# Kernel optimization log

Hardware: AMD Instinct MI355X
Metric: run time of the kernel (lower is better)

The kernel has to match this reference:

```python
import jax, jax.numpy as jnp
import numpy as np

D_MODEL = 2048
NUM_HEADS = 16
HEAD_DIM = D_MODEL // NUM_HEADS


def setup_inputs() -> dict:
    key = jax.random.key(0)
    ks = jax.random.split(key, 11)
    B, S = 2, 2048
    scale = 1.0 / np.sqrt(D_MODEL)
    inp = {
        "q": jax.random.normal(ks[0], (B, S, D_MODEL), jnp.float32),
        "k": jax.random.normal(ks[1], (B, S, D_MODEL), jnp.float32),
        "v": jax.random.normal(ks[2], (B, S, D_MODEL), jnp.float32),
        "Wq": jax.random.normal(ks[3], (D_MODEL, D_MODEL), jnp.float32) * scale,
        "bq": jnp.zeros((D_MODEL,), jnp.float32),
        "Wk": jax.random.normal(ks[4], (D_MODEL, D_MODEL), jnp.float32) * scale,
        "bk": jnp.zeros((D_MODEL,), jnp.float32),
        "Wv": jax.random.normal(ks[5], (D_MODEL, D_MODEL), jnp.float32) * scale,
        "bv": jnp.zeros((D_MODEL,), jnp.float32),
        "Wo": jax.random.normal(ks[6], (D_MODEL, D_MODEL), jnp.float32) * scale,
        "bo": jnp.zeros((D_MODEL,), jnp.float32),
    }
    return inp


def reference(q, k, v, Wq, bq, Wk, bk, Wv, bv, Wo, bo):
    B, S, _ = q.shape
    # projections (torch Linear: x @ W.T + b)
    qh = (q @ Wq.T + bq).reshape(B, S, NUM_HEADS, HEAD_DIM).transpose(0, 2, 1, 3)
    kh = (k @ Wk.T + bk).reshape(B, S, NUM_HEADS, HEAD_DIM).transpose(0, 2, 1, 3)
    vh = (v @ Wv.T + bv).reshape(B, S, NUM_HEADS, HEAD_DIM).transpose(0, 2, 1, 3)
    # scaled dot-product attention, full O(S^2) scores as in original
    scores = jnp.einsum("bhqd,bhkd->bhqk", qh, kh) / jnp.sqrt(
        jnp.asarray(HEAD_DIM, jnp.float32)
    )
    attn = jax.nn.softmax(scores, axis=-1)
    out = jnp.einsum("bhqk,bhkd->bhqd", attn, vh)
    out = out.transpose(0, 2, 1, 3).reshape(B, S, D_MODEL)
    return out @ Wo.T + bo
```

## Files before the change

### kernel.cpp

```cpp
#include <hip/hip_runtime.h>


typedef __attribute__((ext_vector_type(8))) short bf16x8;
typedef __attribute__((ext_vector_type(4))) float f32x4;
typedef __attribute__((ext_vector_type(8))) unsigned short u16x8;

__device__ __forceinline__ unsigned short f2bf(float f) {
  unsigned int u = __float_as_uint(f);
  u += 0x7fffu + ((u >> 16) & 1u);
  return (unsigned short)(u >> 16);
}

#if __has_builtin(__builtin_amdgcn_cvt_pk_bf16_f32)
__device__ __forceinline__ unsigned int pack2bf(float x, float y) {
  auto r = __builtin_amdgcn_cvt_pk_bf16_f32(x, y);
  return __builtin_bit_cast(unsigned int, r);
}
#else
__device__ __forceinline__ unsigned int pack2bf(float x, float y) {
  return (unsigned int)f2bf(x) | ((unsigned int)f2bf(y) << 16);
}
#endif

__device__ __forceinline__ float fast_exp2(float x) {
#if __has_builtin(__builtin_amdgcn_exp2f)
  return __builtin_amdgcn_exp2f(x);
#else
  return exp2f(x);
#endif
}

__device__ __forceinline__ void async16(const void* g, void* l) {
  __builtin_amdgcn_global_load_lds(
      (const __attribute__((address_space(1))) unsigned int*)g,
      (__attribute__((address_space(3))) unsigned int*)l, 16, 0, 0);
}

__device__ __forceinline__ f32x4 mfma_bf16(bf16x8 a, bf16x8 b, f32x4 c) {
  return __builtin_amdgcn_mfma_f32_16x16x32_bf16(a, b, c, 0, 0, 0);
}

__global__ __launch_bounds__(256) void cvt_kernel(
    const float* __restrict__ q, const float* __restrict__ k,
    const float* __restrict__ v, const float* __restrict__ Wq,
    const float* __restrict__ Wk, const float* __restrict__ Wv,
    const float* __restrict__ Wo, unsigned short* __restrict__ Xq,
    unsigned short* __restrict__ Xk, unsigned short* __restrict__ Xv,
    unsigned short* __restrict__ WqB, unsigned short* __restrict__ WkB,
    unsigned short* __restrict__ WvB, unsigned short* __restrict__ WoB) {
  size_t i = ((size_t)blockIdx.x * 256 + threadIdx.x) * 8;
  const float* src;
  unsigned short* dst;
  size_t off;
  if (i < 8388608ull) { src = q; dst = Xq; off = i; }
  else if (i < 16777216ull) { src = k; dst = Xk; off = i - 8388608ull; }
  else if (i < 25165824ull) { src = v; dst = Xv; off = i - 16777216ull; }
  else if (i < 29360128ull) { src = Wq; dst = WqB; off = i - 25165824ull; }
  else if (i < 33554432ull) { src = Wk; dst = WkB; off = i - 29360128ull; }
  else if (i < 37748736ull) { src = Wv; dst = WvB; off = i - 33554432ull; }
  else { src = Wo; dst = WoB; off = i - 37748736ull; }
  f32x4 a = *(const f32x4*)(src + off);
  f32x4 b = *(const f32x4*)(src + off + 4);
  u16x8 r;
  r[0] = f2bf(a[0]); r[1] = f2bf(a[1]); r[2] = f2bf(a[2]); r[3] = f2bf(a[3]);
  r[4] = f2bf(b[0]); r[5] = f2bf(b[1]); r[6] = f2bf(b[2]); r[7] = f2bf(b[3]);
  *(u16x8*)(dst + off) = r;
}

__device__ __forceinline__ void gemm_core_k2048(
    const unsigned short* __restrict__ A, const unsigned short* __restrict__ Bm,
    int m0, int n0, unsigned short* As, unsigned short* Bs,
    f32x4 (&acc)[4][4]) {
  const int tid = threadIdx.x;
  const int lane = tid & 63;
  const int wave = tid >> 6;
  const int quad = lane >> 4;
  const int l15 = lane & 15;
  const int wmt = (wave >> 1) * 4;
  const int wnt = (wave & 1) * 4;
  const int K = 2048;

  auto stage = [&](int kt, int buf) {
    unsigned short* SA = As + buf * (128 * 64);
    unsigned short* SB = Bs + buf * (128 * 64);
#pragma unroll
    for (int p = 0; p < 4; ++p) {
      int x = p * 256 + tid;
      int row = ((x >> 7) << 4) + ((x >> 3) & 15);
      int gk = kt + (((x & 7) ^ ((x >> 3) & 7)) << 3);
      async16(A + (size_t)(m0 + row) * K + gk,
              (char*)SA + (size_t)(p * 256 + wave * 64) * 16);
      async16(Bm + (size_t)(n0 + row) * K + gk,
              (char*)SB + (size_t)(p * 256 + wave * 64) * 16);
    }
  };
  stage(0, 0);
#pragma unroll 1
  for (int it = 0; it < 32; ++it) {
    __syncthreads();
    if (it + 1 < 32) stage((it + 1) * 64, (it + 1) & 1);
    const unsigned short* SA = As + (it & 1) * (128 * 64);
    const unsigned short* SB = Bs + (it & 1) * (128 * 64);
#pragma unroll
    for (int s = 0; s < 2; ++s) {
      const int cs = (s * 4 + quad) ^ (l15 & 7);
      bf16x8 af[4], bfr[4];
#pragma unroll
      for (int t = 0; t < 4; ++t) {
        af[t] = *(const bf16x8*)(SA + ((wmt + t) * 128 + l15 * 8 + cs) * 8);
        bfr[t] = *(const bf16x8*)(SB + ((wnt + t) * 128 + l15 * 8 + cs) * 8);
      }
#pragma unroll
      for (int mt = 0; mt < 4; ++mt)
#pragma unroll
        for (int nt = 0; nt < 4; ++nt)
          acc[mt][nt] = mfma_bf16(af[mt], bfr[nt], acc[mt][nt]);
    }
  }
}

__global__ __launch_bounds__(256, 2) void qkv_gemm(
    const unsigned short* __restrict__ Xq, const unsigned short* __restrict__ Xk,
    const unsigned short* __restrict__ Xv, const unsigned short* __restrict__ Wq,
    const unsigned short* __restrict__ Wk, const unsigned short* __restrict__ Wv,
    const float* __restrict__ bq, const float* __restrict__ bk,
    const float* __restrict__ bv, unsigned short* __restrict__ Qb,
    unsigned short* __restrict__ Kb, unsigned short* __restrict__ Vt) {
  __shared__ unsigned short As[2][128 * 64];
  __shared__ unsigned short Bs[2][128 * 64];
  const int z = blockIdx.z;
  const unsigned short* A = z == 0 ? Xq : z == 1 ? Xk : Xv;
  const unsigned short* Bm = z == 0 ? Wq : z == 1 ? Wk : Wv;
  const float* bias = z == 0 ? bq : z == 1 ? bk : bv;
  const int m0 = blockIdx.y * 128;
  const int n0 = blockIdx.x * 128;

  f32x4 acc[4][4];
#pragma unroll
  for (int i = 0; i < 4; ++i)
#pragma unroll
    for (int j = 0; j < 4; ++j) acc[i][j] = f32x4{0.f, 0.f, 0.f, 0.f};
  gemm_core_k2048(A, Bm, m0, n0, As[0], Bs[0], acc);

  const int lane = threadIdx.x & 63;
  const int wave = threadIdx.x >> 6;
  const int quad = lane >> 4;
  const int l15 = lane & 15;
  const int wmt = (wave >> 1) * 4;
  const int wnt = (wave & 1) * 4;
  const float SK = z == 0 ? 0.12753102331285527f : 1.0f;
  const int N = 2048;

#pragma unroll
  for (int nt = 0; nt < 4; ++nt) {
    int col = n0 + (wnt + nt) * 16 + l15;
    float bv_ = bias[col];
    if (z == 2) {
      int h = col >> 7, d = col & 127;
#pragma unroll
      for (int mt = 0; mt < 4; ++mt) {
        int row0 = m0 + (wmt + mt) * 16 + quad * 4;
        int bb = row0 >> 11, s = row0 & 2047;
        uint2 pk;
        pk.x = pack2bf(acc[mt][nt][0] + bv_, acc[mt][nt][1] + bv_);
        pk.y = pack2bf(acc[mt][nt][2] + bv_, acc[mt][nt][3] + bv_);
        *(uint2*)(Vt + ((size_t)((bb * 16 + h) * 128 + d)) * 2048 + s) = pk;
      }
    } else {
      unsigned short* C = z == 0 ? Qb : Kb;
#pragma unroll
      for (int mt = 0; mt < 4; ++mt) {
        int row0 = m0 + (wmt + mt) * 16 + quad * 4;
#pragma unroll
        for (int r = 0; r < 4; ++r)
          C[(size_t)(row0 + r) * N + col] = f2bf((acc[mt][nt][r] + bv_) * SK);
      }
    }
  }
}

__global__ __launch_bounds__(256, 2) void o_gemm(
    const unsigned short* __restrict__ A, const unsigned short* __restrict__ Bm,
    const float* __restrict__ bias, float* __restrict__ Cf) {
  __shared__ unsigned short As[2][128 * 64];
  __shared__ unsigned short Bs[2][128 * 64];
  const int m0 = blockIdx.y * 128;
  const int n0 = blockIdx.x * 128;

  f32x4 acc[4][4];
#pragma unroll
  for (int i = 0; i < 4; ++i)
#pragma unroll
    for (int j = 0; j < 4; ++j) acc[i][j] = f32x4{0.f, 0.f, 0.f, 0.f};
  gemm_core_k2048(A, Bm, m0, n0, As[0], Bs[0], acc);

  const int lane = threadIdx.x & 63;
  const int wave = threadIdx.x >> 6;
  const int quad = lane >> 4;
  const int l15 = lane & 15;
  const int wmt = (wave >> 1) * 4;
  const int wnt = (wave & 1) * 4;
  const int N = 2048;
#pragma unroll
  for (int nt = 0; nt < 4; ++nt) {
    int col = n0 + (wnt + nt) * 16 + l15;
    float bv_ = bias[col];
#pragma unroll
    for (int mt = 0; mt < 4; ++mt) {
      int row0 = m0 + (wmt + mt) * 16 + quad * 4;
#pragma unroll
      for (int r = 0; r < 4; ++r)
        Cf[(size_t)(row0 + r) * N + col] = acc[mt][nt][r] + bv_;
    }
  }
}

__global__ __launch_bounds__(256, 2) void attn_kernel(
    const unsigned short* __restrict__ Qg, const unsigned short* __restrict__ Kg,
    const unsigned short* __restrict__ Vt, unsigned short* __restrict__ ctx) {
  __shared__ unsigned short Ks[2][64 * 128];
  __shared__ unsigned short Vs[2][128 * 64];
  __shared__ unsigned short Ps[128 * 64];
  const int tid = threadIdx.x;
  const int lane = tid & 63;
  const int wave = tid >> 6;
  const int quad = lane >> 4;
  const int l15 = lane & 15;
  const int qt = blockIdx.x, h = blockIdx.y, b = blockIdx.z;
  const int q0 = qt * 128;
  const int swz = (l15 & 7) * 8;

  bf16x8 aq[2][4];
#pragma unroll
  for (int mt = 0; mt < 2; ++mt) {
    const unsigned short* qrow =
        Qg + (size_t)(b * 2048 + q0 + wave * 32 + mt * 16 + l15) * 2048 + h * 128;
#pragma unroll
    for (int ks = 0; ks < 4; ++ks)
      aq[mt][ks] = *(const bf16x8*)(qrow + ks * 32 + quad * 8);
  }

  f32x4 o[2][8];
#pragma unroll
  for (int mt = 0; mt < 2; ++mt)
#pragma unroll
    for (int dt = 0; dt < 8; ++dt) o[mt][dt] = f32x4{0.f, 0.f, 0.f, 0.f};
  f32x4 lacc[2] = {f32x4{0.f, 0.f, 0.f, 0.f}, f32x4{0.f, 0.f, 0.f, 0.f}};

  auto stage = [&](int t, int buf) {
#pragma unroll
    for (int p = 0; p < 4; ++p) {
      int slot = p * 256 + tid;
      {
        int nt = slot >> 8, c = (slot >> 4) & 15, r15 = slot & 15;
        const unsigned short* g =
            Kg + (size_t)(b * 2048 + t * 64 + nt * 16 + r15) * 2048 + h * 128 + c * 8;
        async16(g, (char*)Ks[buf] + (size_t)(p * 256 + wave * 64) * 16);
      }
      {
        int dt = slot >> 7, c = (slot >> 4) & 7, n15 = slot & 15;
        const unsigned short* g =
            Vt + ((size_t)(b * 16 + h) * 128 + dt * 16 + n15) * 2048 + t * 64 + c * 8;
        async16(g, (char*)Vs[buf] + (size_t)(p * 256 + wave * 64) * 16);
      }
    }
  };
  stage(0, 0);

  for (int t = 0; t < 32; ++t) {
    __syncthreads();
    if (t + 1 < 32) stage(t + 1, (t + 1) & 1);
    const unsigned short* Kb = Ks[t & 1];
    const unsigned short* Vb = Vs[t & 1];

    f32x4 sc[2][4];
#pragma unroll
    for (int nt = 0; nt < 4; ++nt) {
      sc[0][nt] = f32x4{0.f, 0.f, 0.f, 0.f};
      sc[1][nt] = f32x4{0.f, 0.f, 0.f, 0.f};
#pragma unroll
      for (int ks = 0; ks < 4; ++ks) {
        bf16x8 bk = *(const bf16x8*)(Kb + (nt * 256 + (ks * 4 + quad) * 16 + l15) * 8);
        sc[0][nt] = mfma_bf16(bk, aq[0][ks], sc[0][nt]);
        sc[1][nt] = mfma_bf16(bk, aq[1][ks], sc[1][nt]);
      }
    }

#pragma unroll
    for (int mt = 0; mt < 2; ++mt) {
      int prow = (wave * 32 + mt * 16 + l15) * 64;
#pragma unroll
      for (int nt = 0; nt < 4; ++nt) {
        f32x4 p;
#pragma unroll
        for (int r = 0; r < 4; ++r) p[r] = fast_exp2(sc[mt][nt][r]);
        lacc[mt] += p;
        uint2 pk;
        pk.x = pack2bf(p[0], p[1]);
        pk.y = pack2bf(p[2], p[3]);
        *(uint2*)(Ps + prow + ((nt * 16 + quad * 4) ^ swz)) = pk;
      }
    }

    bf16x8 ap[2][2];
#pragma unroll
    for (int mt = 0; mt < 2; ++mt) {
      int prow = (wave * 32 + mt * 16 + l15) * 64;
#pragma unroll
      for (int ks = 0; ks < 2; ++ks)
        ap[mt][ks] = *(const bf16x8*)(Ps + prow + ((ks * 32 + quad * 8) ^ swz));
    }
#pragma unroll
    for (int dt = 0; dt < 8; ++dt) {
#pragma unroll
      for (int ks = 0; ks < 2; ++ks) {
        bf16x8 bv = *(const bf16x8*)(Vb + (dt * 128 + (ks * 4 + quad) * 16 + l15) * 8);
        o[0][dt] = mfma_bf16(ap[0][ks], bv, o[0][dt]);
        o[1][dt] = mfma_bf16(ap[1][ks], bv, o[1][dt]);
      }
    }
  }

  float lq[2];
#pragma unroll
  for (int mt = 0; mt < 2; ++mt) {
    float s = lacc[mt][0] + lacc[mt][1] + lacc[mt][2] + lacc[mt][3];
    s += __shfl_xor(s, 16, 64);
    s += __shfl_xor(s, 32, 64);
    lq[mt] = s;
  }

#pragma unroll
  for (int mt = 0; mt < 2; ++mt) {
#pragma unroll
    for (int r = 0; r < 4; ++r) {
      float lr = __shfl(lq[mt], quad * 4 + r, 64);
      float inv = 1.0f / lr;
      unsigned short* crow =
          ctx + (size_t)(b * 2048 + q0 + wave * 32 + mt * 16 + quad * 4 + r) * 2048 +
          h * 128;
#pragma unroll
      for (int dt = 0; dt < 8; ++dt)
        crow[dt * 16 + l15] = f2bf(o[mt][dt][r] * inv);
    }
  }
}

extern "C" void kernel_launch(void* const* d_in, const int* in_sizes, int n_in,
                              void* d_out, int out_size, void* d_ws,
                              size_t ws_size, hipStream_t stream) {
  const float* q = (const float*)d_in[0];
  const float* k = (const float*)d_in[1];
  const float* v = (const float*)d_in[2];
  const float* Wq = (const float*)d_in[3];
  const float* bq = (const float*)d_in[4];
  const float* Wk = (const float*)d_in[5];
  const float* bk = (const float*)d_in[6];
  const float* Wv = (const float*)d_in[7];
  const float* bv = (const float*)d_in[8];
  const float* Wo = (const float*)d_in[9];
  const float* bo = (const float*)d_in[10];
  float* out = (float*)d_out;

  char* ws = (char*)d_ws;
  const size_t MB = 1024 * 1024;
  unsigned short* Xq  = (unsigned short*)(ws + 0 * MB);
  unsigned short* Xk  = (unsigned short*)(ws + 16 * MB);
  unsigned short* Xv  = (unsigned short*)(ws + 32 * MB);
  unsigned short* WqB = (unsigned short*)(ws + 48 * MB);
  unsigned short* WkB = (unsigned short*)(ws + 56 * MB);
  unsigned short* WvB = (unsigned short*)(ws + 64 * MB);
  unsigned short* WoB = (unsigned short*)(ws + 72 * MB);
  unsigned short* Qb  = (unsigned short*)(ws + 80 * MB);
  unsigned short* Kb  = (unsigned short*)(ws + 96 * MB);
  unsigned short* Vt  = (unsigned short*)(ws + 112 * MB);
  unsigned short* ctx = Xq;

  cvt_kernel<<<20480, 256, 0, stream>>>(q, k, v, Wq, Wk, Wv, Wo, Xq, Xk, Xv,
                                        WqB, WkB, WvB, WoB);
  qkv_gemm<<<dim3(16, 32, 3), 256, 0, stream>>>(Xq, Xk, Xv, WqB, WkB, WvB, bq,
                                                bk, bv, Qb, Kb, Vt);
  attn_kernel<<<dim3(16, 16, 2), 256, 0, stream>>>(Qb, Kb, Vt, ctx);
  o_gemm<<<dim3(16, 32), 256, 0, stream>>>(ctx, WoB, bo, out);
}
```

Measured before the change: 452.9 us.

## Replace QKV projection GEMM with 256x256-tile, 8-wave pipelined kernel

The QKV projection kernel now uses 256x256 output tiles with 512 threads, in place of 128x128 tiles with 256 threads. The K-loop is software-pipelined: global loads for four 128-row sub-tiles are staggered across phases, LDS fragment reads are double-buffered in registers, and MFMA phases are raised in priority with setprio. The aim is more data reuse per LDS byte, less global traffic, and memory latency hidden behind MFMA work. In exchange, the grid shrinks to 384 blocks, register pressure from 128 accumulators is high, and the per-phase barriers add synchronization overhead.

```diff
diff --git a/kernel.cpp b/kernel.cpp
--- a/kernel.cpp
+++ b/kernel.cpp
@@ -67,6 +67,184 @@
   *(u16x8*)(dst + off) = r;
 }
 
+#define MFMA_PHASE(AF, MB)                                                    \
+  do {                                                                        \
+    __builtin_amdgcn_s_setprio(1);                                            \
+    _Pragma("unroll") for (int ks = 0; ks < 2; ++ks) {                        \
+      _Pragma("unroll") for (int m2 = 0; m2 < 2; ++m2) {                      \
+        _Pragma("unroll") for (int nt = 0; nt < 4; ++nt) {                    \
+          acc[(MB) + m2][nt] =                                                \
+              mfma_bf16(AF[m2][ks], Bf[nt][ks], acc[(MB) + m2][nt]);          \
+        }                                                                     \
+      }                                                                       \
+    }                                                                         \
+    __builtin_amdgcn_s_setprio(0);                                            \
+  } while (0)
+
+__global__ __launch_bounds__(512, 2) void qkv_gemm256(
+    const unsigned short* __restrict__ Xq, const unsigned short* __restrict__ Xk,
+    const unsigned short* __restrict__ Xv, const unsigned short* __restrict__ Wq,
+    const unsigned short* __restrict__ Wk, const unsigned short* __restrict__ Wv,
+    const float* __restrict__ bq, const float* __restrict__ bk,
+    const float* __restrict__ bv, unsigned short* __restrict__ Qb,
+    unsigned short* __restrict__ Kb, unsigned short* __restrict__ Vt) {
+  __shared__ unsigned short S[2][4][128 * 64];
+  const int z = blockIdx.z;
+  const unsigned short* A = z == 0 ? Xq : z == 1 ? Xk : Xv;
+  const unsigned short* Bm = z == 0 ? Wq : z == 1 ? Wk : Wv;
+  const float* bias = z == 0 ? bq : z == 1 ? bk : bv;
+  const int m0 = blockIdx.y * 256;
+  const int n0 = blockIdx.x * 256;
+  const int tid = threadIdx.x;
+  const int lane = tid & 63;
+  const int wave = tid >> 6;
+  const int quad = lane >> 4;
+  const int l15 = lane & 15;
+  const int wm = wave >> 2;
+  const int wn = wave & 3;
+  const int cxor = l15 & 7;
+  const int K = 2048;
+
+  auto stage = [&](int r, int kt, int buf) {
+#pragma unroll
+    for (int p = 0; p < 2; ++p) {
+      int x = p * 512 + tid;
+      int row = ((x >> 7) << 4) + ((x >> 3) & 15);
+      int gk = kt * 64 + (((x & 7) ^ ((x >> 3) & 7)) << 3);
+      const unsigned short* src =
+          (r < 2) ? Bm + (size_t)(n0 + r * 128 + row) * K + gk
+                  : A + (size_t)(m0 + (r - 2) * 128 + row) * K + gk;
+      async16(src, (char*)S[buf][r] + (size_t)(p * 512 + wave * 64) * 16);
+    }
+  };
+  auto rdA = [&](int buf, int mt, int ks) -> bf16x8 {
+    const unsigned short* base = S[buf][2 + wm];
+    int chunk = mt * 128 + l15 * 8 + ((ks * 4 + quad) ^ cxor);
+    return *(const bf16x8*)(base + chunk * 8);
+  };
+  auto rdB = [&](int buf, int nt, int ks) -> bf16x8 {
+    const unsigned short* base = S[buf][wn >> 1];
+    int chunk = ((wn & 1) * 4 + nt) * 128 + l15 * 8 + ((ks * 4 + quad) ^ cxor);
+    return *(const bf16x8*)(base + chunk * 8);
+  };
+
+  f32x4 acc[8][4];
+#pragma unroll
+  for (int i = 0; i < 8; ++i)
+#pragma unroll
+    for (int j = 0; j < 4; ++j) acc[i][j] = f32x4{0.f, 0.f, 0.f, 0.f};
+  bf16x8 Bf[4][2], AX[2][2], AY[2][2];
+
+  stage(0, 0, 0); stage(1, 0, 0); stage(2, 0, 0); stage(3, 0, 0);
+  stage(0, 1, 1); stage(1, 1, 1); stage(2, 1, 1);
+  asm volatile("s_waitcnt vmcnt(6)" ::: "memory");
+  __builtin_amdgcn_s_barrier();
+#pragma unroll
+  for (int nt = 0; nt < 4; ++nt)
+#pragma unroll
+    for (int ks = 0; ks < 2; ++ks) Bf[nt][ks] = rdB(0, nt, ks);
+#pragma unroll
+  for (int ks = 0; ks < 2; ++ks) {
+    AX[0][ks] = rdA(0, 0, ks);
+    AX[1][ks] = rdA(0, 1, ks);
+  }
+
+#pragma unroll 1
+  for (int t = 0; t < 32; ++t) {
+    const int buf = t & 1;
+    const int nbuf = buf ^ 1;
+    if (t < 31) stage(3, t + 1, nbuf);
+#pragma unroll
+    for (int ks = 0; ks < 2; ++ks) {
+      AY[0][ks] = rdA(buf, 2, ks);
+      AY[1][ks] = rdA(buf, 3, ks);
+    }
+    __builtin_amdgcn_sched_barrier(0);
+    __builtin_amdgcn_s_barrier();
+    __builtin_amdgcn_sched_barrier(0);
+    MFMA_PHASE(AX, 0);
+    __builtin_amdgcn_sched_barrier(0);
+    __builtin_amdgcn_s_barrier();
+    if (t < 30) stage(0, t + 2, buf);
+#pragma unroll
+    for (int ks = 0; ks < 2; ++ks) {
+      AX[0][ks] = rdA(buf, 4, ks);
+      AX[1][ks] = rdA(buf, 5, ks);
+    }
+    __builtin_amdgcn_sched_barrier(0);
+    __builtin_amdgcn_s_barrier();
+    __builtin_amdgcn_sched_barrier(0);
+    MFMA_PHASE(AY, 2);
+    __builtin_amdgcn_sched_barrier(0);
+    __builtin_amdgcn_s_barrier();
+    if (t < 30) stage(1, t + 2, buf);
+#pragma unroll
+    for (int ks = 0; ks < 2; ++ks) {
+      AY[0][ks] = rdA(buf, 6, ks);
+      AY[1][ks] = rdA(buf, 7, ks);
+    }
+    __builtin_amdgcn_sched_barrier(0);
+    __builtin_amdgcn_s_barrier();
+    __builtin_amdgcn_sched_barrier(0);
+    MFMA_PHASE(AX, 4);
+    if (t < 30) {
+      asm volatile("s_waitcnt vmcnt(4)" ::: "memory");
+    } else if (t == 30) {
+      asm volatile("s_waitcnt vmcnt(0)" ::: "memory");
+    }
+    __builtin_amdgcn_sched_barrier(0);
+    __builtin_amdgcn_s_barrier();
+    if (t < 30) stage(2, t + 2, buf);
+    if (t < 31) {
+#pragma unroll
+      for (int ks = 0; ks < 2; ++ks) {
+        AX[0][ks] = rdA(nbuf, 0, ks);
+        AX[1][ks] = rdA(nbuf, 1, ks);
+      }
+    }
+    __builtin_amdgcn_sched_barrier(0);
+    __builtin_amdgcn_s_barrier();
+    __builtin_amdgcn_sched_barrier(0);
+    MFMA_PHASE(AY, 6);
+    if (t < 31) {
+#pragma unroll
+      for (int nt = 0; nt < 4; ++nt)
+#pragma unroll
+        for (int ks = 0; ks < 2; ++ks) Bf[nt][ks] = rdB(nbuf, nt, ks);
+    }
+    __builtin_amdgcn_sched_barrier(0);
+    __builtin_amdgcn_s_barrier();
+  }
+
+  const float SK = z == 0 ? 0.12753102331285527f : 1.0f;
+#pragma unroll
+  for (int nt = 0; nt < 4; ++nt) {
+    int col = n0 + wn * 64 + nt * 16 + l15;
+    float bv_ = bias[col];
+    if (z == 2) {
+      int h = col >> 7, d = col & 127;
+#pragma unroll
+      for (int mt = 0; mt < 8; ++mt) {
+        int row0 = m0 + wm * 128 + mt * 16 + quad * 4;
+        int bb = row0 >> 11, s = row0 & 2047;
+        uint2 pk;
+        pk.x = pack2bf(acc[mt][nt][0] + bv_, acc[mt][nt][1] + bv_);
+        pk.y = pack2bf(acc[mt][nt][2] + bv_, acc[mt][nt][3] + bv_);
+        *(uint2*)(Vt + ((size_t)((bb * 16 + h) * 128 + d)) * 2048 + s) = pk;
+      }
+    } else {
+      unsigned short* C = z == 0 ? Qb : Kb;
+#pragma unroll
+      for (int mt = 0; mt < 8; ++mt) {
+        int row0 = m0 + wm * 128 + mt * 16 + quad * 4;
+#pragma unroll
+        for (int r = 0; r < 4; ++r)
+          C[(size_t)(row0 + r) * 2048 + col] = f2bf((acc[mt][nt][r] + bv_) * SK);
+      }
+    }
+  }
+}
+
 __device__ __forceinline__ void gemm_core_k2048(
     const unsigned short* __restrict__ A, const unsigned short* __restrict__ Bm,
     int m0, int n0, unsigned short* As, unsigned short* Bs,
@@ -115,66 +293,6 @@
 #pragma unroll
         for (int nt = 0; nt < 4; ++nt)
           acc[mt][nt] = mfma_bf16(af[mt], bfr[nt], acc[mt][nt]);
-    }
-  }
-}
-
-__global__ __launch_bounds__(256, 2) void qkv_gemm(
-    const unsigned short* __restrict__ Xq, const unsigned short* __restrict__ Xk,
-    const unsigned short* __restrict__ Xv, const unsigned short* __restrict__ Wq,
-    const unsigned short* __restrict__ Wk, const unsigned short* __restrict__ Wv,
-    const float* __restrict__ bq, const float* __restrict__ bk,
-    const float* __restrict__ bv, unsigned short* __restrict__ Qb,
-    unsigned short* __restrict__ Kb, unsigned short* __restrict__ Vt) {
-  __shared__ unsigned short As[2][128 * 64];
-  __shared__ unsigned short Bs[2][128 * 64];
-  const int z = blockIdx.z;
-  const unsigned short* A = z == 0 ? Xq : z == 1 ? Xk : Xv;
-  const unsigned short* Bm = z == 0 ? Wq : z == 1 ? Wk : Wv;
-  const float* bias = z == 0 ? bq : z == 1 ? bk : bv;
-  const int m0 = blockIdx.y * 128;
-  const int n0 = blockIdx.x * 128;
-
-  f32x4 acc[4][4];
-#pragma unroll
-  for (int i = 0; i < 4; ++i)
-#pragma unroll
-    for (int j = 0; j < 4; ++j) acc[i][j] = f32x4{0.f, 0.f, 0.f, 0.f};
-  gemm_core_k2048(A, Bm, m0, n0, As[0], Bs[0], acc);
-
-  const int lane = threadIdx.x & 63;
-  const int wave = threadIdx.x >> 6;
-  const int quad = lane >> 4;
-  const int l15 = lane & 15;
-  const int wmt = (wave >> 1) * 4;
-  const int wnt = (wave & 1) * 4;
-  const float SK = z == 0 ? 0.12753102331285527f : 1.0f;
-  const int N = 2048;
-
-#pragma unroll
-  for (int nt = 0; nt < 4; ++nt) {
-    int col = n0 + (wnt + nt) * 16 + l15;
-    float bv_ = bias[col];
-    if (z == 2) {
-      int h = col >> 7, d = col & 127;
-#pragma unroll
-      for (int mt = 0; mt < 4; ++mt) {
-        int row0 = m0 + (wmt + mt) * 16 + quad * 4;
-        int bb = row0 >> 11, s = row0 & 2047;
-        uint2 pk;
-        pk.x = pack2bf(acc[mt][nt][0] + bv_, acc[mt][nt][1] + bv_);
-        pk.y = pack2bf(acc[mt][nt][2] + bv_, acc[mt][nt][3] + bv_);
-        *(uint2*)(Vt + ((size_t)((bb * 16 + h) * 128 + d)) * 2048 + s) = pk;
-      }
-    } else {
-      unsigned short* C = z == 0 ? Qb : Kb;
-#pragma unroll
-      for (int mt = 0; mt < 4; ++mt) {
-        int row0 = m0 + (wmt + mt) * 16 + quad * 4;
-#pragma unroll
-        for (int r = 0; r < 4; ++r)
-          C[(size_t)(row0 + r) * N + col] = f2bf((acc[mt][nt][r] + bv_) * SK);
-      }
     }
   }
 }
@@ -378,8 +496,8 @@
 
   cvt_kernel<<<20480, 256, 0, stream>>>(q, k, v, Wq, Wk, Wv, Wo, Xq, Xk, Xv,
                                         WqB, WkB, WvB, WoB);
-  qkv_gemm<<<dim3(16, 32, 3), 256, 0, stream>>>(Xq, Xk, Xv, WqB, WkB, WvB, bq,
-                                                bk, bv, Qb, Kb, Vt);
+  qkv_gemm256<<<dim3(8, 16, 3), 512, 0, stream>>>(Xq, Xk, Xv, WqB, WkB, WvB,
+                                                  bq, bk, bv, Qb, Kb, Vt);
   attn_kernel<<<dim3(16, 16, 2), 256, 0, stream>>>(Qb, Kb, Vt, ctx);
   o_gemm<<<dim3(16, 32), 256, 0, stream>>>(ctx, WoB, bo, out);
 }
```

After: 474.7 us. +4.8%, slower.

## Rewrite QKV GEMM with two-wave 128x128 tiles and add MFMA priority hints

Applied to the files above, without the earlier changes.

The QKV projection GEMM is rewritten to use 128 threads (2 waves), each computing a 128x64 sub-tile with 8x4 MFMA accumulators. It uses a K-step of 32 with a 64-iteration double-buffered async load and a new swizzled LDS layout. This raises per-wave register reuse of A fragments and reduces LDS traffic per MFMA, at the cost of more accumulator registers and fewer waves per block. Separately, the attention kernel wraps its MFMA sections in s_setprio so those waves get scheduling priority over waves doing softmax work.

```diff
diff --git a/kernel.cpp b/kernel.cpp
--- a/kernel.cpp
+++ b/kernel.cpp
@@ -67,6 +67,109 @@
   *(u16x8*)(dst + off) = r;
 }
 
+__global__ __launch_bounds__(128, 2) void qkv_gemm(
+    const unsigned short* __restrict__ Xq, const unsigned short* __restrict__ Xk,
+    const unsigned short* __restrict__ Xv, const unsigned short* __restrict__ Wq,
+    const unsigned short* __restrict__ Wk, const unsigned short* __restrict__ Wv,
+    const float* __restrict__ bq, const float* __restrict__ bk,
+    const float* __restrict__ bv, unsigned short* __restrict__ Qb,
+    unsigned short* __restrict__ Kb, unsigned short* __restrict__ Vt) {
+  __shared__ unsigned short S[2][2][4096];
+  const int z = blockIdx.z;
+  const unsigned short* A = z == 0 ? Xq : z == 1 ? Xk : Xv;
+  const unsigned short* Bm = z == 0 ? Wq : z == 1 ? Wk : Wv;
+  const float* bias = z == 0 ? bq : z == 1 ? bk : bv;
+  const int m0 = blockIdx.y * 128;
+  const int n0 = blockIdx.x * 128;
+  const int tid = threadIdx.x;
+  const int lane = tid & 63;
+  const int w = tid >> 6;
+  const int quad = lane >> 4;
+  const int l15 = lane & 15;
+  const int K = 2048;
+
+  const unsigned short* gsrcA[4];
+  const unsigned short* gsrcB[4];
+#pragma unroll
+  for (int p = 0; p < 4; ++p) {
+    int s = p * 128 + tid;
+    int j = s >> 3;
+    int oc2 = (s & 7) ^ (j & 7);
+    int row = j * 2 + (oc2 & 1);
+    int oct = oc2 >> 1;
+    gsrcA[p] = A + (size_t)(m0 + row) * K + oct * 8;
+    gsrcB[p] = Bm + (size_t)(n0 + row) * K + oct * 8;
+  }
+  auto stage = [&](int buf) {
+#pragma unroll
+    for (int p = 0; p < 4; ++p)
+      async16(gsrcA[p], (char*)S[buf][0] + (size_t)(p * 128 + tid) * 16);
+#pragma unroll
+    for (int p = 0; p < 4; ++p)
+      async16(gsrcB[p], (char*)S[buf][1] + (size_t)(p * 128 + tid) * 16);
+#pragma unroll
+    for (int p = 0; p < 4; ++p) { gsrcA[p] += 32; gsrcB[p] += 32; }
+  };
+
+  const int lbyte = (l15 >> 1) * 128 +
+                    (((quad << 1) | (l15 & 1)) ^ ((l15 >> 1) & 7)) * 16;
+
+  f32x4 acc[8][4];
+#pragma unroll
+  for (int i = 0; i < 8; ++i)
+#pragma unroll
+    for (int j = 0; j < 4; ++j) acc[i][j] = f32x4{0.f, 0.f, 0.f, 0.f};
+
+  stage(0);
+#pragma unroll 2
+  for (int t = 0; t < 64; ++t) {
+    __syncthreads();
+    if (t + 1 < 64) stage((t + 1) & 1);
+    const char* SA = (const char*)S[t & 1][0];
+    const char* SB = (const char*)S[t & 1][1];
+    bf16x8 af[8], bf[4];
+#pragma unroll
+    for (int mt = 0; mt < 8; ++mt)
+      af[mt] = *(const bf16x8*)(SA + mt * 1024 + lbyte);
+#pragma unroll
+    for (int nt = 0; nt < 4; ++nt)
+      bf[nt] = *(const bf16x8*)(SB + (w * 4 + nt) * 1024 + lbyte);
+#pragma unroll
+    for (int mt = 0; mt < 8; ++mt)
+#pragma unroll
+      for (int nt = 0; nt < 4; ++nt)
+        acc[mt][nt] = mfma_bf16(af[mt], bf[nt], acc[mt][nt]);
+  }
+
+  const float SK = z == 0 ? 0.12753102331285527f : 1.0f;
+#pragma unroll
+  for (int nt = 0; nt < 4; ++nt) {
+    int col = n0 + w * 64 + nt * 16 + l15;
+    float bv_ = bias[col];
+    if (z == 2) {
+      int h = col >> 7, d = col & 127;
+#pragma unroll
+      for (int mt = 0; mt < 8; ++mt) {
+        int row0 = m0 + mt * 16 + quad * 4;
+        int bb = row0 >> 11, s = row0 & 2047;
+        uint2 pk;
+        pk.x = pack2bf(acc[mt][nt][0] + bv_, acc[mt][nt][1] + bv_);
+        pk.y = pack2bf(acc[mt][nt][2] + bv_, acc[mt][nt][3] + bv_);
+        *(uint2*)(Vt + ((size_t)((bb * 16 + h) * 128 + d)) * 2048 + s) = pk;
+      }
+    } else {
+      unsigned short* C = z == 0 ? Qb : Kb;
+#pragma unroll
+      for (int mt = 0; mt < 8; ++mt) {
+        int row0 = m0 + mt * 16 + quad * 4;
+#pragma unroll
+        for (int r = 0; r < 4; ++r)
+          C[(size_t)(row0 + r) * 2048 + col] = f2bf((acc[mt][nt][r] + bv_) * SK);
+      }
+    }
+  }
+}
+
 __device__ __forceinline__ void gemm_core_k2048(
     const unsigned short* __restrict__ A, const unsigned short* __restrict__ Bm,
     int m0, int n0, unsigned short* As, unsigned short* Bs,
@@ -115,66 +218,6 @@
 #pragma unroll
         for (int nt = 0; nt < 4; ++nt)
           acc[mt][nt] = mfma_bf16(af[mt], bfr[nt], acc[mt][nt]);
-    }
-  }
-}
-
-__global__ __launch_bounds__(256, 2) void qkv_gemm(
-    const unsigned short* __restrict__ Xq, const unsigned short* __restrict__ Xk,
-    const unsigned short* __restrict__ Xv, const unsigned short* __restrict__ Wq,
-    const unsigned short* __restrict__ Wk, const unsigned short* __restrict__ Wv,
-    const float* __restrict__ bq, const float* __restrict__ bk,
-    const float* __restrict__ bv, unsigned short* __restrict__ Qb,
-    unsigned short* __restrict__ Kb, unsigned short* __restrict__ Vt) {
-  __shared__ unsigned short As[2][128 * 64];
-  __shared__ unsigned short Bs[2][128 * 64];
-  const int z = blockIdx.z;
-  const unsigned short* A = z == 0 ? Xq : z == 1 ? Xk : Xv;
-  const unsigned short* Bm = z == 0 ? Wq : z == 1 ? Wk : Wv;
-  const float* bias = z == 0 ? bq : z == 1 ? bk : bv;
-  const int m0 = blockIdx.y * 128;
-  const int n0 = blockIdx.x * 128;
-
-  f32x4 acc[4][4];
-#pragma unroll
-  for (int i = 0; i < 4; ++i)
-#pragma unroll
-    for (int j = 0; j < 4; ++j) acc[i][j] = f32x4{0.f, 0.f, 0.f, 0.f};
-  gemm_core_k2048(A, Bm, m0, n0, As[0], Bs[0], acc);
-
-  const int lane = threadIdx.x & 63;
-  const int wave = threadIdx.x >> 6;
-  const int quad = lane >> 4;
-  const int l15 = lane & 15;
-  const int wmt = (wave >> 1) * 4;
-  const int wnt = (wave & 1) * 4;
-  const float SK = z == 0 ? 0.12753102331285527f : 1.0f;
-  const int N = 2048;
-
-#pragma unroll
-  for (int nt = 0; nt < 4; ++nt) {
-    int col = n0 + (wnt + nt) * 16 + l15;
-    float bv_ = bias[col];
-    if (z == 2) {
-      int h = col >> 7, d = col & 127;
-#pragma unroll
-      for (int mt = 0; mt < 4; ++mt) {
-        int row0 = m0 + (wmt + mt) * 16 + quad * 4;
-        int bb = row0 >> 11, s = row0 & 2047;
-        uint2 pk;
-        pk.x = pack2bf(acc[mt][nt][0] + bv_, acc[mt][nt][1] + bv_);
-        pk.y = pack2bf(acc[mt][nt][2] + bv_, acc[mt][nt][3] + bv_);
-        *(uint2*)(Vt + ((size_t)((bb * 16 + h) * 128 + d)) * 2048 + s) = pk;
-      }
-    } else {
-      unsigned short* C = z == 0 ? Qb : Kb;
-#pragma unroll
-      for (int mt = 0; mt < 4; ++mt) {
-        int row0 = m0 + (wmt + mt) * 16 + quad * 4;
-#pragma unroll
-        for (int r = 0; r < 4; ++r)
-          C[(size_t)(row0 + r) * N + col] = f2bf((acc[mt][nt][r] + bv_) * SK);
-      }
     }
   }
 }
@@ -274,6 +317,7 @@
     const unsigned short* Vb = Vs[t & 1];
 
     f32x4 sc[2][4];
+    __builtin_amdgcn_s_setprio(1);
 #pragma unroll
     for (int nt = 0; nt < 4; ++nt) {
       sc[0][nt] = f32x4{0.f, 0.f, 0.f, 0.f};
@@ -285,6 +329,7 @@
         sc[1][nt] = mfma_bf16(bk, aq[1][ks], sc[1][nt]);
       }
     }
+    __builtin_amdgcn_s_setprio(0);
 
 #pragma unroll
     for (int mt = 0; mt < 2; ++mt) {
@@ -310,6 +355,7 @@
       for (int ks = 0; ks < 2; ++ks)
         ap[mt][ks] = *(const bf16x8*)(Ps + prow + ((ks * 32 + quad * 8) ^ swz));
     }
+    __builtin_amdgcn_s_setprio(1);
 #pragma unroll
     for (int dt = 0; dt < 8; ++dt) {
 #pragma unroll
@@ -319,6 +365,7 @@
         o[1][dt] = mfma_bf16(ap[1][ks], bv, o[1][dt]);
       }
     }
+    __builtin_amdgcn_s_setprio(0);
   }
 
   float lq[2];
@@ -378,7 +425,7 @@
 
   cvt_kernel<<<20480, 256, 0, stream>>>(q, k, v, Wq, Wk, Wv, Wo, Xq, Xk, Xv,
                                         WqB, WkB, WvB, WoB);
-  qkv_gemm<<<dim3(16, 32, 3), 256, 0, stream>>>(Xq, Xk, Xv, WqB, WkB, WvB, bq,
+  qkv_gemm<<<dim3(16, 32, 3), 128, 0, stream>>>(Xq, Xk, Xv, WqB, WkB, WvB, bq,
                                                 bk, bv, Qb, Kb, Vt);
   attn_kernel<<<dim3(16, 16, 2), 256, 0, stream>>>(Qb, Kb, Vt, ctx);
   o_gemm<<<dim3(16, 32), 256, 0, stream>>>(ctx, WoB, bo, out);
```

Result: slower. 482.4 us (+6.5%).
